# Optimization experiments

Hardware: AMD Instinct MI355X
Metric: run time of the kernel (lower is better)

Reference implementation:

```python
import jax, jax.numpy as jnp
import numpy as np

N_NEURONS = 2048
IN_DIM = 1024
OUT_DIM = 1024
TOKENS = 4096
TIME_STEPS = 3
DENSITY = 0.25


def setup_inputs() -> dict:
    key = jax.random.key(0)
    ks = jax.random.split(key, 10)
    x = jax.random.normal(ks[0], (TOKENS, IN_DIM), dtype=jnp.float32)
    W_in = jax.random.normal(ks[1], (N_NEURONS, IN_DIM), dtype=jnp.float32) * (1.0 / np.sqrt(IN_DIM))
    b_in = jax.random.normal(ks[2], (N_NEURONS,), dtype=jnp.float32) * 0.01
    weights = jax.random.normal(ks[3], (N_NEURONS, N_NEURONS), dtype=jnp.float32) * 0.3
    J = jax.random.normal(ks[4], (N_NEURONS, N_NEURONS), dtype=jnp.float32) * 0.1
    theta = jax.random.uniform(ks[5], (N_NEURONS,), dtype=jnp.float32) * 1.0 + 0.25
    lam = jnp.asarray(0.35, dtype=jnp.float32)
    # connection mask: rand < density, zero diagonal (buffer, fixed)
    m = (jax.random.uniform(ks[6], (N_NEURONS, N_NEURONS)) < DENSITY).astype(jnp.float32)
    mask = m * (1.0 - jnp.eye(N_NEURONS, dtype=jnp.float32))
    noise_raw = jax.random.normal(ks[7], (TIME_STEPS, TOKENS, N_NEURONS), dtype=jnp.float32)
    W_out = jax.random.normal(ks[8], (OUT_DIM, N_NEURONS), dtype=jnp.float32) * (1.0 / np.sqrt(N_NEURONS))
    b_out = jax.random.normal(ks[9], (OUT_DIM,), dtype=jnp.float32) * 0.01
    return {"x": x, "W_in": W_in, "b_in": b_in, "weights": weights, "J": J,
            "theta": theta, "lam": lam, "mask": mask, "noise_raw": noise_raw,
            "W_out": W_out, "b_out": b_out, "time_steps": TIME_STEPS}


def reference(x, W_in, b_in, weights, J, theta, lam, mask, noise_raw, W_out, b_out, time_steps):
    # input projection: [tokens, in_dim] -> [tokens, n]
    state = x @ W_in.T + b_in
    eff_w = weights * mask          # [n, n]
    J_m = J * mask                  # [n, n]
    T = jnp.abs(jnp.sin(2.0 * theta))  # temperature [n]
    for t in range(time_steps):
        signal = state @ eff_w                     # [tokens, n]
        s = jnp.tanh(state)
        # einsum('bi,ij,bj->bj', s, J_m, s) == (s @ J_m) * s
        delta = (s @ J_m) * s                      # [tokens, n]
        noise = noise_raw[t] * T * 0.1             # [tokens, n]
        state = jnp.tanh(signal + lam * delta + noise)
    return state @ W_out.T + b_out
```

## Files before the change

### kernel.cpp

```cpp
#include <hip/hip_runtime.h>
#include <hip/hip_fp16.h>

#define TOKENS 4096
#define NN 2048
#define IN_DIM 1024
#define OUT_DIM 1024
#define TSTEPS 3

typedef _Float16 half8 __attribute__((ext_vector_type(8)));
typedef _Float16 half4 __attribute__((ext_vector_type(4)));
typedef float f32x4 __attribute__((ext_vector_type(4)));

__device__ __forceinline__ void gload_lds16(const void* g, void* l) {
    __builtin_amdgcn_global_load_lds(
        (const __attribute__((address_space(1))) unsigned*)g,
        (__attribute__((address_space(3))) unsigned*)l, 16, 0, 0);
}

__global__ __launch_bounds__(512, 2)
void dual_gemm(const _Float16* __restrict__ A0, const _Float16* __restrict__ B0,
               float* __restrict__ C0,
               const _Float16* __restrict__ A1, const _Float16* __restrict__ B1,
               float* __restrict__ C1)
{
    __shared__ __align__(16) _Float16 lds[4 * 16384];
    const int tid  = threadIdx.x;
    const int wid  = tid >> 6;
    const int lane = tid & 63;

    int bid = blockIdx.x;
    const int g = bid >> 7;
    bid &= 127;
    const int bx = bid & 7;
    const int by = bid >> 3;
    const _Float16* __restrict__ A = g ? A1 : A0;
    const _Float16* __restrict__ B = g ? B1 : B0;
    float* __restrict__ C = g ? C1 : C0;
    const int brow = by << 8;
    const int bcol = bx << 8;

    const int sr = tid >> 2;
    const int sc = ((tid & 3) ^ ((tid >> 3) & 3)) << 3;
    const _Float16* gA = A + (size_t)(brow + sr) * NN + sc;
    const _Float16* gB = B + (size_t)(bcol + sr) * NN + sc;
    const int ldst = wid << 9;

    auto stage = [&](int u) {
        _Float16* l = lds + (u & 3) * 16384;
        const _Float16* a = gA + u * 32;
        const _Float16* b = gB + u * 32;
        gload_lds16(a,            l + ldst);
        gload_lds16(a + 128 * NN, l + 4096  + ldst);
        gload_lds16(b,            l + 8192  + ldst);
        gload_lds16(b + 128 * NN, l + 12288 + ldst);
    };

    const int wr = (wid >> 2) << 7;
    const int wc = (wid & 3) << 6;
    const int lr = lane & 15;
    const int swz = ((lane >> 4) ^ ((lr >> 1) & 3)) << 3;
    const int aRd = (wr + lr) * 32 + swz;
    const int bRd = 8192 + (wc + lr) * 32 + swz;

    f32x4 acc[8][4];
#pragma unroll
    for (int m = 0; m < 8; ++m)
#pragma unroll
        for (int n = 0; n < 4; ++n) acc[m][n] = (f32x4){0.f, 0.f, 0.f, 0.f};

    stage(0); stage(1); stage(2);

    for (int t = 0; t < 64; ++t) {
        if (t < 61) {
            stage(t + 3);
            asm volatile("s_waitcnt vmcnt(12)" ::: "memory");
        } else if (t == 61) {
            asm volatile("s_waitcnt vmcnt(8)" ::: "memory");
        } else if (t == 62) {
            asm volatile("s_waitcnt vmcnt(4)" ::: "memory");
        } else {
            asm volatile("s_waitcnt vmcnt(0)" ::: "memory");
        }
        __builtin_amdgcn_s_barrier();
        asm volatile("" ::: "memory");
        __builtin_amdgcn_sched_barrier(0);

        const _Float16* lb = lds + (t & 3) * 16384;
        half8 bf[4];
#pragma unroll
        for (int n = 0; n < 4; ++n)
            bf[n] = *(const half8*)&lb[bRd + (n << 9)];
        __builtin_amdgcn_s_setprio(1);
#pragma unroll
        for (int m = 0; m < 8; ++m) {
            half8 af = *(const half8*)&lb[aRd + (m << 9)];
#pragma unroll
            for (int n = 0; n < 4; ++n)
                acc[m][n] = __builtin_amdgcn_mfma_f32_16x16x32_f16(af, bf[n], acc[m][n], 0, 0, 0);
        }
        __builtin_amdgcn_s_setprio(0);
        __builtin_amdgcn_sched_barrier(0);
        asm volatile("" ::: "memory");
        __builtin_amdgcn_s_barrier();
    }

    const int cr = (lane >> 4) << 2;
    const int cc = lane & 15;
#pragma unroll
    for (int m = 0; m < 8; ++m) {
#pragma unroll
        for (int n = 0; n < 4; ++n) {
            const size_t o0 = (size_t)(brow + wr + m * 16 + cr) * NN
                            + (bcol + wc + n * 16 + cc);
#pragma unroll
            for (int j = 0; j < 4; ++j)
                C[o0 + (size_t)j * NN] = acc[m][n][j];
        }
    }
}

template<int EPI>
__global__ __launch_bounds__(256)
void gemm_bt(const _Float16* __restrict__ A, const _Float16* __restrict__ B,
             float* __restrict__ C, const float* __restrict__ bias,
             _Float16* __restrict__ oSta, _Float16* __restrict__ oS,
             int M, int N, int K)
{
    __shared__ _Float16 As[128 * 32];
    __shared__ _Float16 Bs[128 * 32];
    const int tid  = threadIdx.x;
    const int wid  = tid >> 6;
    const int lane = tid & 63;
    const int wr = (wid >> 1) * 64;
    const int wc = (wid & 1) * 64;
    const int brow = blockIdx.y * 128;
    const int bcol = blockIdx.x * 128;

    f32x4 acc[4][4];
#pragma unroll
    for (int m = 0; m < 4; ++m)
#pragma unroll
        for (int n = 0; n < 4; ++n) acc[m][n] = (f32x4){0.f, 0.f, 0.f, 0.f};

    const int ldr = tid >> 2;
    const int ldc = (tid & 3) * 8;
    const int wbase = (wid << 4) * 32;
    const int kq = (lane >> 4) * 8;
    const int lr = lane & 15;

    for (int k0 = 0; k0 < K; k0 += 32) {
        __syncthreads();
        gload_lds16(A + (size_t)(brow + ldr) * K + k0 + ldc, As + wbase);
        gload_lds16(A + (size_t)(brow + 64 + ldr) * K + k0 + ldc, As + 64 * 32 + wbase);
        gload_lds16(B + (size_t)(bcol + ldr) * K + k0 + ldc, Bs + wbase);
        gload_lds16(B + (size_t)(bcol + 64 + ldr) * K + k0 + ldc, Bs + 64 * 32 + wbase);
        __syncthreads();

        half8 af[4], bf[4];
#pragma unroll
        for (int m = 0; m < 4; ++m)
            af[m] = *(const half8*)&As[(wr + m * 16 + lr) * 32 + kq];
#pragma unroll
        for (int n = 0; n < 4; ++n)
            bf[n] = *(const half8*)&Bs[(wc + n * 16 + lr) * 32 + kq];
#pragma unroll
        for (int m = 0; m < 4; ++m)
#pragma unroll
            for (int n = 0; n < 4; ++n)
                acc[m][n] = __builtin_amdgcn_mfma_f32_16x16x32_f16(af[m], bf[n], acc[m][n], 0, 0, 0);
    }

    const int cr = (lane >> 4) * 4;
    const int cc = lane & 15;
#pragma unroll
    for (int m = 0; m < 4; ++m) {
#pragma unroll
        for (int n = 0; n < 4; ++n) {
            const int ccol = bcol + wc + n * 16 + cc;
#pragma unroll
            for (int j = 0; j < 4; ++j) {
                const int crow = brow + wr + m * 16 + cr + j;
                float v = acc[m][n][j];
                const size_t o = (size_t)crow * N + ccol;
                if (EPI == 1) {
                    v += bias[ccol];
                    oSta[o] = (_Float16)v;
                    oS[o] = (_Float16)tanhf(v);
                } else {
                    C[o] = v + bias[ccol];
                }
            }
        }
    }
}

__global__ void cvt_f16(const float* __restrict__ in, _Float16* __restrict__ out, int n4) {
    int i = blockIdx.x * blockDim.x + threadIdx.x;
    if (i < n4) {
        f32x4 v = *(const f32x4*)&in[(size_t)i * 4];
        half4 h;
        h[0] = (_Float16)v[0]; h[1] = (_Float16)v[1];
        h[2] = (_Float16)v[2]; h[3] = (_Float16)v[3];
        *(half4*)&out[(size_t)i * 4] = h;
    }
}

__global__ void transmul2(const float* __restrict__ W, const float* __restrict__ J,
                          const float* __restrict__ Mk,
                          _Float16* __restrict__ effT, _Float16* __restrict__ JmT) {
    __shared__ float tw[32][33];
    __shared__ float tj[32][33];
    const int bx = blockIdx.x * 32, by = blockIdx.y * 32;
    const int tx = threadIdx.x, ty0 = threadIdx.y;
#pragma unroll
    for (int r = 0; r < 4; ++r) {
        int ty = ty0 + r * 8;
        size_t idx = (size_t)(by + ty) * NN + bx + tx;
        float mv = Mk[idx];
        tw[ty][tx] = W[idx] * mv;
        tj[ty][tx] = J[idx] * mv;
    }
    __syncthreads();
#pragma unroll
    for (int r = 0; r < 4; ++r) {
        int ty = ty0 + r * 8;
        size_t o = (size_t)(bx + ty) * NN + by + tx;
        effT[o] = (_Float16)tw[tx][ty];
        JmT[o]  = (_Float16)tj[tx][ty];
    }
}

__global__ void tsc_kernel(const float* __restrict__ theta, float* __restrict__ Tsc) {
    int i = blockIdx.x * blockDim.x + threadIdx.x;
    if (i < NN) Tsc[i] = fabsf(sinf(2.0f * theta[i])) * 0.1f;
}

__global__ void step_kernel(const float* __restrict__ signal, const float* __restrict__ sJ,
                            const float* __restrict__ noise, const float* __restrict__ Tsc,
                            const float* __restrict__ lamp,
                            _Float16* __restrict__ stateH, _Float16* __restrict__ sH) {
    const int i4 = blockIdx.x * blockDim.x + threadIdx.x;
    const float lam = lamp[0];
    const size_t base = (size_t)i4 * 4;
    f32x4 sg = *(const f32x4*)&signal[base];
    f32x4 dj = *(const f32x4*)&sJ[base];
    f32x4 nz = *(const f32x4*)&noise[base];
    const int col4 = (int)(base & (NN - 1));
    f32x4 tv = *(const f32x4*)&Tsc[col4];
    half4 so = *(const half4*)&sH[base];
    half4 hs, hn;
#pragma unroll
    for (int j = 0; j < 4; ++j) {
        float s = (float)so[j];
        float arg = sg[j] + lam * (dj[j] * s) + nz[j] * tv[j];
        float st = tanhf(arg);
        hs[j] = (_Float16)st;
        hn[j] = (_Float16)tanhf(st);
    }
    *(half4*)&stateH[base] = hs;
    *(half4*)&sH[base] = hn;
}

extern "C" void kernel_launch(void* const* d_in, const int* in_sizes, int n_in,
                              void* d_out, int out_size, void* d_ws, size_t ws_size,
                              hipStream_t stream) {
    const float* x       = (const float*)d_in[0];
    const float* W_in    = (const float*)d_in[1];
    const float* b_in    = (const float*)d_in[2];
    const float* weights = (const float*)d_in[3];
    const float* Jmat    = (const float*)d_in[4];
    const float* theta   = (const float*)d_in[5];
    const float* lam     = (const float*)d_in[6];
    const float* mask    = (const float*)d_in[7];
    const float* noise   = (const float*)d_in[8];
    const float* W_out   = (const float*)d_in[9];
    const float* b_out   = (const float*)d_in[10];
    float* out = (float*)d_out;

    char* w = (char*)d_ws;
    auto alloc = [&](size_t b) { char* p = w; w += (b + 255) & ~(size_t)255; return p; };
    _Float16* xh     = (_Float16*)alloc((size_t)TOKENS * IN_DIM * 2);
    _Float16* WinH   = (_Float16*)alloc((size_t)NN * IN_DIM * 2);
    _Float16* WoutH  = (_Float16*)alloc((size_t)OUT_DIM * NN * 2);
    _Float16* effT   = (_Float16*)alloc((size_t)NN * NN * 2);
    _Float16* JmT    = (_Float16*)alloc((size_t)NN * NN * 2);
    _Float16* stateH = (_Float16*)alloc((size_t)TOKENS * NN * 2);
    _Float16* sH     = (_Float16*)alloc((size_t)TOKENS * NN * 2);
    float* Tsc       = (float*)alloc((size_t)NN * 4);
    float* signal    = (float*)alloc((size_t)TOKENS * NN * 4);
    float* sJ        = (float*)alloc((size_t)TOKENS * NN * 4);

    cvt_f16<<<TOKENS * IN_DIM / 4 / 256, 256, 0, stream>>>(x, xh, TOKENS * IN_DIM / 4);
    cvt_f16<<<NN * IN_DIM / 4 / 256, 256, 0, stream>>>(W_in, WinH, NN * IN_DIM / 4);
    cvt_f16<<<OUT_DIM * NN / 4 / 256, 256, 0, stream>>>(W_out, WoutH, OUT_DIM * NN / 4);
    transmul2<<<dim3(NN / 32, NN / 32), dim3(32, 8), 0, stream>>>(weights, Jmat, mask, effT, JmT);
    tsc_kernel<<<NN / 256, 256, 0, stream>>>(theta, Tsc);

    gemm_bt<1><<<dim3(NN / 128, TOKENS / 128), 256, 0, stream>>>(
        xh, WinH, nullptr, b_in, stateH, sH, TOKENS, NN, IN_DIM);

    for (int t = 0; t < TSTEPS; ++t) {
        dual_gemm<<<256, 512, 0, stream>>>(stateH, effT, signal, sH, JmT, sJ);
        step_kernel<<<TOKENS * NN / 4 / 256, 256, 0, stream>>>(
            signal, sJ, noise + (size_t)t * TOKENS * NN, Tsc, lam, stateH, sH);
    }

    gemm_bt<2><<<dim3(OUT_DIM / 128, TOKENS / 128), 256, 0, stream>>>(
        stateH, WoutH, out, b_out, nullptr, nullptr, TOKENS, OUT_DIM, NN);
}
```

Baseline: 413.2 us.

## Split GEMM k-step into two half-phases interleaving A/B prefetch with MFMA

Restructures the main loop of the dual GEMM so each k-step runs in two phases: first the fragments for rows 0-3 are read from LDS and the A tile prefetch is issued, then rows 4-7 are read and the B tile prefetch is issued. Global-to-LDS loads are spread across the MFMA work and the wait for the next stage moves to the end of the iteration. The aim is to overlap memory issue with compute, in the style of ping-pong scheduling. It adds extra barriers per iteration and relies on vmcnt counts staying correct for the four-deep buffer ring, which is delicate.

```diff
diff --git a/kernel.cpp b/kernel.cpp
--- a/kernel.cpp
+++ b/kernel.cpp
@@ -45,12 +45,15 @@
     const _Float16* gB = B + (size_t)(bcol + sr) * NN + sc;
     const int ldst = wid << 9;
 
-    auto stage = [&](int u) {
+    auto stageA = [&](int u) {
         _Float16* l = lds + (u & 3) * 16384;
         const _Float16* a = gA + u * 32;
+        gload_lds16(a,            l + ldst);
+        gload_lds16(a + 128 * NN, l + 4096 + ldst);
+    };
+    auto stageB = [&](int u) {
+        _Float16* l = lds + (u & 3) * 16384;
         const _Float16* b = gB + u * 32;
-        gload_lds16(a,            l + ldst);
-        gload_lds16(a + 128 * NN, l + 4096  + ldst);
         gload_lds16(b,            l + 8192  + ldst);
         gload_lds16(b + 128 * NN, l + 12288 + ldst);
     };
@@ -68,39 +71,53 @@
 #pragma unroll
         for (int n = 0; n < 4; ++n) acc[m][n] = (f32x4){0.f, 0.f, 0.f, 0.f};
 
-    stage(0); stage(1); stage(2);
+    stageA(0); stageB(0); stageA(1); stageB(1); stageA(2); stageB(2);
+    asm volatile("s_waitcnt vmcnt(8)" ::: "memory");
+    __builtin_amdgcn_s_barrier();
 
     for (int t = 0; t < 64; ++t) {
-        if (t < 61) {
-            stage(t + 3);
-            asm volatile("s_waitcnt vmcnt(12)" ::: "memory");
-        } else if (t == 61) {
-            asm volatile("s_waitcnt vmcnt(8)" ::: "memory");
-        } else if (t == 62) {
-            asm volatile("s_waitcnt vmcnt(4)" ::: "memory");
-        } else {
-            asm volatile("s_waitcnt vmcnt(0)" ::: "memory");
-        }
-        __builtin_amdgcn_s_barrier();
-        asm volatile("" ::: "memory");
-        __builtin_amdgcn_sched_barrier(0);
-
         const _Float16* lb = lds + (t & 3) * 16384;
-        half8 bf[4];
+
+        half8 af[4], bf[4];
+#pragma unroll
+        for (int m = 0; m < 4; ++m)
+            af[m] = *(const half8*)&lb[aRd + (m << 9)];
 #pragma unroll
         for (int n = 0; n < 4; ++n)
             bf[n] = *(const half8*)&lb[bRd + (n << 9)];
+        if (t < 61) stageA(t + 3);
+        __builtin_amdgcn_s_barrier();
+        asm volatile("s_waitcnt lgkmcnt(0)" ::: "memory");
+        __builtin_amdgcn_sched_barrier(0);
         __builtin_amdgcn_s_setprio(1);
 #pragma unroll
-        for (int m = 0; m < 8; ++m) {
-            half8 af = *(const half8*)&lb[aRd + (m << 9)];
+        for (int m = 0; m < 4; ++m)
 #pragma unroll
             for (int n = 0; n < 4; ++n)
-                acc[m][n] = __builtin_amdgcn_mfma_f32_16x16x32_f16(af, bf[n], acc[m][n], 0, 0, 0);
-        }
+                acc[m][n] = __builtin_amdgcn_mfma_f32_16x16x32_f16(af[m], bf[n], acc[m][n], 0, 0, 0);
         __builtin_amdgcn_s_setprio(0);
         __builtin_amdgcn_sched_barrier(0);
-        asm volatile("" ::: "memory");
+        __builtin_amdgcn_s_barrier();
+
+#pragma unroll
+        for (int m = 0; m < 4; ++m)
+            af[m] = *(const half8*)&lb[aRd + ((m + 4) << 9)];
+        if (t < 61) stageB(t + 3);
+        __builtin_amdgcn_s_barrier();
+        asm volatile("s_waitcnt lgkmcnt(0)" ::: "memory");
+        __builtin_amdgcn_sched_barrier(0);
+        __builtin_amdgcn_s_setprio(1);
+#pragma unroll
+        for (int m = 0; m < 4; ++m)
+#pragma unroll
+            for (int n = 0; n < 4; ++n)
+                acc[m + 4][n] = __builtin_amdgcn_mfma_f32_16x16x32_f16(af[m], bf[n], acc[m + 4][n], 0, 0, 0);
+        __builtin_amdgcn_s_setprio(0);
+        __builtin_amdgcn_sched_barrier(0);
+
+        if (t < 61)      asm volatile("s_waitcnt vmcnt(8)" ::: "memory");
+        else if (t == 61) asm volatile("s_waitcnt vmcnt(4)" ::: "memory");
+        else if (t == 62) asm volatile("s_waitcnt vmcnt(0)" ::: "memory");
         __builtin_amdgcn_s_barrier();
     }
 
```

Result: faster. 391.8 us (-5.2%).
